# Optimization experiments

Measured on AMD Instinct MI355X. Metric: run time of the kernel, lower is better.

Reference implementation:

```python
import jax, jax.numpy as jnp
import numpy as np

D_MODEL = 384
NUM_CODES = 256
BETAS = (0.05, 0.25, 0.6)
B = 8192


def _vq(x, codebook, beta):
    """Standard EMA-VQ forward: nearest-code lookup + straight-through + commitment loss.
    x: (B, N, D), codebook: (K, D).
    (EMA buffer updates are training-time, no-grad side effects and are omitted.)"""
    flat = x.reshape(-1, x.shape[-1])  # (B*N, D)
    d2 = (jnp.sum(flat * flat, axis=-1, keepdims=True)
          - 2.0 * flat @ codebook.T
          + jnp.sum(codebook * codebook, axis=-1))  # (B*N, K)
    idx = jnp.argmin(d2, axis=-1)                    # (B*N,)
    q_hard = codebook[idx].reshape(x.shape)          # gather (B, N, D)
    idx = idx.reshape(x.shape[:-1])                  # (B, N)
    loss = beta * jnp.mean(jnp.square(jax.lax.stop_gradient(q_hard) - x))
    q = x + jax.lax.stop_gradient(q_hard - x)        # straight-through estimator
    return q, loss, idx


def setup_inputs() -> dict:
    key = jax.random.key(0)
    k0, k1, k2, k3, k4, k5 = jax.random.split(key, 6)
    return {
        "l0_feats": jax.random.normal(k0, (B, 4, D_MODEL), dtype=jnp.float32),
        "l1_feats": jax.random.normal(k1, (B, 16, D_MODEL), dtype=jnp.float32),
        "l2_feats": jax.random.normal(k2, (B, 16, D_MODEL), dtype=jnp.float32),
        "codebook0": jax.random.normal(k3, (NUM_CODES, D_MODEL), dtype=jnp.float32),
        "codebook1": jax.random.normal(k4, (NUM_CODES, D_MODEL), dtype=jnp.float32),
        "codebook2": jax.random.normal(k5, (NUM_CODES, D_MODEL), dtype=jnp.float32),
    }


def reference(l0_feats, l1_feats, l2_feats, codebook0, codebook1, codebook2):
    q0, loss0, idx0 = _vq(l0_feats, codebook0, BETAS[0])
    q1, loss1, idx1 = _vq(l1_feats, codebook1, BETAS[1])
    q2, loss2, idx2 = _vq(l2_feats, codebook2, BETAS[2])
    total_vq_loss = loss0 + loss1 + loss2
    return (idx0, idx1, idx2, total_vq_loss, q0, q1, q2)
```

## Files before the change

### kernel.cpp

```cpp
#include <hip/hip_runtime.h>


typedef _Float16 half8 __attribute__((ext_vector_type(8)));
typedef float f32x16 __attribute__((ext_vector_type(16)));

#define D_MODEL 384
#define NSEG 96
#define NKT 12
#define BM 64
#define RTAU 0.004f

__device__ __forceinline__ float4 ld4(const float* p) { return *(const float4*)p; }

__device__ __forceinline__ void cvt8(const float4& a, const float4& b, half8& hi, half8& lo) {
  const float v[8] = {a.x, a.y, a.z, a.w, b.x, b.y, b.z, b.w};
#pragma unroll
  for (int u = 0; u < 8; ++u) {
    _Float16 h = (_Float16)v[u];
    hi[u] = h;
    lo[u] = (_Float16)(v[u] - (float)h);
  }
}

__device__ __forceinline__ void gload_lds16(const void* g, void* l) {
  __builtin_amdgcn_global_load_lds(
      (const __attribute__((address_space(1))) unsigned int*)g,
      (__attribute__((address_space(3))) unsigned int*)l, 16, 0, 0);
}

__global__ __launch_bounds__(64) void vq_norms(const float* __restrict__ c0,
                                               const float* __restrict__ c1,
                                               const float* __restrict__ c2,
                                               float* __restrict__ en,
                                               int* __restrict__ counts) {
  if (blockIdx.x == 0 && threadIdx.x < 4) counts[threadIdx.x] = 0;
  const int row = blockIdx.x;
  const float* cb = (row < 256) ? c0 : ((row < 512) ? c1 : c2);
  const int n = row & 255;
  const int lane = threadIdx.x;
  const float* r = cb + (size_t)n * D_MODEL;
  float s = 0.f;
  for (int c = lane; c < D_MODEL; c += 64) s = fmaf(r[c], r[c], s);
  for (int m = 1; m < 64; m <<= 1) s += __shfl_xor(s, m, 64);
  if (lane == 0) en[row] = s;
}

__global__ __launch_bounds__(256) void vq_split_cb(const float* __restrict__ c0,
                                                   const float* __restrict__ c1,
                                                   const float* __restrict__ c2,
                                                   half8* __restrict__ bh,
                                                   half8* __restrict__ bl) {
  const int t = blockIdx.x * 256 + threadIdx.x;
  const int lvl = t / 12288;
  const int rem = t - lvl * 12288;
  const int kt = rem >> 10;
  const int f = (rem >> 6) & 15;
  const int lane = rem & 63;
  const int code = (f >> 1) * 32 + (lane & 31);
  const int k0 = kt * 32 + (f & 1) * 16 + (lane >> 5) * 8;
  const float* cb = (lvl == 0) ? c0 : ((lvl == 1) ? c1 : c2);
  const float4 a = ld4(cb + code * D_MODEL + k0);
  const float4 b = ld4(cb + code * D_MODEL + k0 + 4);
  half8 hv, lv;
  cvt8(a, b, hv, lv);
  bh[t] = hv;
  bl[t] = lv;
}

__global__ __launch_bounds__(256) void vq_mfma_all(
    const float* __restrict__ l0, const float* __restrict__ l1,
    const float* __restrict__ l2, const float* __restrict__ c0,
    const float* __restrict__ c1, const float* __restrict__ c2,
    const float* __restrict__ en_all,
    const half8* __restrict__ bh_pre, const half8* __restrict__ bl_pre,
    float* __restrict__ out, float* __restrict__ dmin_all,
    float* __restrict__ xn_all,
    int* __restrict__ list0, int* __restrict__ list1, int* __restrict__ list2,
    int* __restrict__ counts) {
  __shared__ __align__(16) unsigned char smem[40960];
  half8* Ah = (half8*)smem;
  half8* Al = (half8*)(smem + 4096);
  float*  scanbuf = (float*)smem;
  float4* red     = (float4*)(smem + 32768);
  float*  en_s    = (float*)(smem + 36864);
  float4* rowres  = (float4*)(smem + 37888);
  float*  xnp     = (float*)(smem + 38912);
  int*    idxs    = (int*)(smem + 39936);

  const int swz = (blockIdx.x & 7) * 576 + (blockIdx.x >> 3);
  int lvl, blk;
  if (swz < 512)       { lvl = 0; blk = swz; }
  else if (swz < 2560) { lvl = 1; blk = swz - 512; }
  else                 { lvl = 2; blk = swz - 2560; }
  const float* x  = (lvl == 0) ? l0 : ((lvl == 1) ? l1 : l2);
  const float* cb = (lvl == 0) ? c0 : ((lvl == 1) ? c1 : c2);
  const float* en = en_all + lvl * 256;
  const half8* bh = bh_pre + lvl * 12288;
  const half8* bl = bl_pre + lvl * 12288;
  const long ioff = (lvl == 0) ? 0 : ((lvl == 1) ? 32768 : 163840);
  float* out_idx = out + ioff;
  float* out_q   = out + ((lvl == 0) ? 294913L : ((lvl == 1) ? 12877825L : 63209473L));
  float* dmin_lvl = dmin_all + ioff;
  float* xn_lvl   = xn_all + ioff;
  int* list = (lvl == 0) ? list0 : ((lvl == 1) ? list1 : list2);
  int* cnt  = counts + lvl;

  const int tid = threadIdx.x;
  const int lane = tid & 63;
  const int w = tid >> 6, wm = w >> 1, wn = w & 1;
  const int c31 = lane & 31, h = lane >> 5;
  const long m0 = (long)blk * BM;

  const int amt = tid >> 7;
  const int akc = (tid >> 6) & 1;
  const float* ap = x + (m0 + amt * 32 + c31) * (long)D_MODEL + akc * 16 + h * 8;
  const int aidx = (amt * 2 + akc) * 64 + lane;

  float4 ra0 = ld4(ap + 0), ra1 = ld4(ap + 4);

  f32x16 acc[4];
#pragma unroll
  for (int n = 0; n < 4; ++n)
#pragma unroll
    for (int i = 0; i < 16; ++i) acc[n][i] = 0.f;

  float xn_part = 0.f;

  for (int kt = 0; kt < NKT; ++kt) {
#pragma unroll
    for (int r = 0; r < 4; ++r) {
      const int f = r * 4 + w;
      const size_t gi = (size_t)kt * 1024 + f * 64 + lane;
      gload_lds16(bh + gi, (void*)(smem + 8192 + f * 1024));
      gload_lds16(bl + gi, (void*)(smem + 24576 + f * 1024));
    }
    {
      half8 hv, lv;
      cvt8(ra0, ra1, hv, lv);
      xn_part = fmaf(ra0.x, ra0.x, xn_part); xn_part = fmaf(ra0.y, ra0.y, xn_part);
      xn_part = fmaf(ra0.z, ra0.z, xn_part); xn_part = fmaf(ra0.w, ra0.w, xn_part);
      xn_part = fmaf(ra1.x, ra1.x, xn_part); xn_part = fmaf(ra1.y, ra1.y, xn_part);
      xn_part = fmaf(ra1.z, ra1.z, xn_part); xn_part = fmaf(ra1.w, ra1.w, xn_part);
      Ah[aidx] = hv; Al[aidx] = lv;
    }
    __syncthreads();

    if (kt + 1 < NKT) {
      const int ko = (kt + 1) * 32;
      ra0 = ld4(ap + ko); ra1 = ld4(ap + ko + 4);
    }
    {
      half8* Bh = (half8*)(smem + 8192);
      half8* Bl = (half8*)(smem + 24576);
      half8 ah0 = Ah[(wm * 2 + 0) * 64 + lane];
      half8 al0 = Al[(wm * 2 + 0) * 64 + lane];
      half8 ah1 = Ah[(wm * 2 + 1) * 64 + lane];
      half8 al1 = Al[(wm * 2 + 1) * 64 + lane];
#pragma unroll
      for (int n = 0; n < 4; ++n) {
        const int nt = wn * 4 + n;
        half8 bh0 = Bh[(nt * 2 + 0) * 64 + lane], bl0 = Bl[(nt * 2 + 0) * 64 + lane];
        half8 bh1 = Bh[(nt * 2 + 1) * 64 + lane], bl1 = Bl[(nt * 2 + 1) * 64 + lane];
        acc[n] = __builtin_amdgcn_mfma_f32_32x32x16_f16(ah0, bh0, acc[n], 0, 0, 0);
        acc[n] = __builtin_amdgcn_mfma_f32_32x32x16_f16(ah0, bl0, acc[n], 0, 0, 0);
        acc[n] = __builtin_amdgcn_mfma_f32_32x32x16_f16(al0, bh0, acc[n], 0, 0, 0);
        acc[n] = __builtin_amdgcn_mfma_f32_32x32x16_f16(ah1, bh1, acc[n], 0, 0, 0);
        acc[n] = __builtin_amdgcn_mfma_f32_32x32x16_f16(ah1, bl1, acc[n], 0, 0, 0);
        acc[n] = __builtin_amdgcn_mfma_f32_32x32x16_f16(al1, bh1, acc[n], 0, 0, 0);
      }
    }
    __syncthreads();
  }

  xnp[(amt * 32 + c31) * 4 + (akc * 2 + h)] = xn_part;
  en_s[tid] = en[tid];

#pragma unroll 1
  for (int b = 0; b < 2; ++b) {
    __syncthreads();
    if (wm == b) {
#pragma unroll
      for (int n = 0; n < 4; ++n) {
        const int colbase = wn * 128 + n * 32 + c31;
#pragma unroll
        for (int rr = 0; rr < 16; ++rr) {
          const int row_b = (rr & 3) + ((rr >> 2) << 3) + (h << 2);
          const int p = colbase ^ ((row_b & 3) << 3);
          scanbuf[row_b * 256 + p] = fmaf(-2.f, acc[n][rr], en_s[colbase]);
        }
      }
    }
    __syncthreads();
    {
      const int srow = tid >> 3, chunk = tid & 7;
      float b1 = 1e30f, b2 = 1e30f; int i1 = 0, i2 = 0;
#pragma unroll
      for (int u = 0; u < 32; ++u) {
        const int col = chunk + u * 8;
        const float d = scanbuf[srow * 256 + (col ^ ((srow & 3) << 3))];
        if (d < b1) { b2 = b1; i2 = i1; b1 = d; i1 = col; }
        else if (d < b2) { b2 = d; i2 = col; }
      }
      red[srow * 8 + chunk] = make_float4(b1, __int_as_float(i1), b2, __int_as_float(i2));
    }
    __syncthreads();
    if (tid < 32) {
      float4 q = red[tid * 8 + 0];
      float fb1 = q.x, fb2 = q.z;
      int fi1 = __float_as_int(q.y), fi2 = __float_as_int(q.w);
#pragma unroll
      for (int c = 1; c < 8; ++c) {
        q = red[tid * 8 + c];
        const float c1 = q.x, c2 = q.z;
        const int j1 = __float_as_int(q.y), j2 = __float_as_int(q.w);
        if (c1 < fb1 || (c1 == fb1 && j1 < fi1)) {
          if (fb1 < c2 || (fb1 == c2 && fi1 < j2)) { fb2 = fb1; fi2 = fi1; }
          else { fb2 = c2; fi2 = j2; }
          fb1 = c1; fi1 = j1;
        } else if (c1 < fb2 || (c1 == fb2 && j1 < fi2)) { fb2 = c1; fi2 = j1; }
      }
      rowres[b * 32 + tid] = make_float4(fb1, __int_as_float(fi1), fb2, __int_as_float(fi2));
    }
  }
  __syncthreads();

  if (tid < BM) {
    const int m = tid;
    const float4 qv = rowres[m];
    const float fb1 = qv.x, fb2 = qv.z;
    const int fi1 = __float_as_int(qv.y);
    const float xn = (xnp[m * 4 + 0] + xnp[m * 4 + 1]) + (xnp[m * 4 + 2] + xnp[m * 4 + 3]);
    idxs[m] = fi1;
    out_idx[m0 + m] = (float)fi1;
    dmin_lvl[m0 + m] = xn + fb1;
    xn_lvl[m0 + m] = xn;
    const bool flg = (fb2 - fb1 < RTAU);
    const unsigned long long mask = __ballot(flg);
    const int nf = __popcll(mask);
    int base = 0;
    if (tid == 0 && nf) base = atomicAdd(cnt, nf);
    base = __shfl(base, 0, 64);
    if (flg) {
      const int pos = __popcll(mask & ((1ull << tid) - 1ull));
      list[base + pos] = (int)(m0 + m);
    }
  }
  __syncthreads();

  float* qb = out_q + m0 * (long)D_MODEL;
  for (int g = tid; g < BM * NSEG; g += 256) {
    const int m = g / NSEG;
    const int seg = g - m * NSEG;
    *(float4*)(qb + m * (long)D_MODEL + seg * 4) = ld4(cb + (long)idxs[m] * D_MODEL + seg * 4);
  }
}

__global__ __launch_bounds__(256) void vq_rescue_all(
    const float* __restrict__ l0, const float* __restrict__ l1,
    const float* __restrict__ l2, const float* __restrict__ c0,
    const float* __restrict__ c1, const float* __restrict__ c2,
    const float* __restrict__ en_all,
    const int* __restrict__ list0, const int* __restrict__ list1,
    const int* __restrict__ list2, const int* __restrict__ counts,
    float* __restrict__ out, float* __restrict__ dmin_all,
    const float* __restrict__ xn_all) {
  __shared__ float xs[8][D_MODEL];
  __shared__ int rows_s[8];
  __shared__ float xns_s[8];
  __shared__ float dall[8][256];
  __shared__ int best_s[8];

  const int lvl = blockIdx.x >> 7;
  const int sb  = blockIdx.x & 127;
  const float* x  = (lvl == 0) ? l0 : ((lvl == 1) ? l1 : l2);
  const float* cb = (lvl == 0) ? c0 : ((lvl == 1) ? c1 : c2);
  const float* en_lvl = en_all + lvl * 256;
  const int* list = (lvl == 0) ? list0 : ((lvl == 1) ? list1 : list2);
  const long ioff = (lvl == 0) ? 0 : ((lvl == 1) ? 32768 : 163840);
  float* out_idx = out + ioff;
  float* out_q   = out + ((lvl == 0) ? 294913L : ((lvl == 1) ? 12877825L : 63209473L));
  float* dmin_lvl = dmin_all + ioff;
  const float* xn_lvl = xn_all + ioff;

  const int tid = threadIdx.x;
  const int count = counts[lvl];
  const int nch = (count + 7) >> 3;
  const float en_t = en_lvl[tid];
  const int w = tid >> 6, lane = tid & 63;
  const float* crow = cb + (long)tid * D_MODEL;

  for (int c = sb; c < nch; c += 128) {
    const int base = c << 3;
    const int R = min(8, count - base);
    if (tid < 8) {
      const int j = min(tid, R - 1);
      const int r = list[base + j];
      rows_s[tid] = r;
      xns_s[tid] = xn_lvl[r];
    }
    __syncthreads();
#pragma unroll
    for (int r = 0; r < 8; ++r)
      if (tid < NSEG) *(float4*)&xs[r][tid * 4] = ld4(x + (long)rows_s[r] * D_MODEL + tid * 4);
    __syncthreads();

    float acc[8] = {0.f, 0.f, 0.f, 0.f, 0.f, 0.f, 0.f, 0.f};
    for (int seg = 0; seg < NSEG; ++seg) {
      const float4 e = ld4(crow + seg * 4);
#pragma unroll
      for (int r = 0; r < 8; ++r) {
        const float4 xv = *(const float4*)&xs[r][seg * 4];
        acc[r] = fmaf(xv.x, e.x, acc[r]);
        acc[r] = fmaf(xv.y, e.y, acc[r]);
        acc[r] = fmaf(xv.z, e.z, acc[r]);
        acc[r] = fmaf(xv.w, e.w, acc[r]);
      }
    }
#pragma unroll
    for (int r = 0; r < 8; ++r)
      dall[r][tid] = fmaf(-2.f, acc[r], xns_s[r]) + en_t;
    __syncthreads();

#pragma unroll
    for (int rr = 0; rr < 2; ++rr) {
      const int r = w + rr * 4;
      if (r < R) {
        float best = dall[r][lane]; int bidx = lane;
#pragma unroll
        for (int u = 1; u < 4; ++u) {
          const int code = lane + u * 64;
          const float d = dall[r][code];
          if (d < best) { best = d; bidx = code; }
        }
        for (int mm = 1; mm < 64; mm <<= 1) {
          const float ov = __shfl_xor(best, mm, 64);
          const int oi = __shfl_xor(bidx, mm, 64);
          if (ov < best || (ov == best && oi < bidx)) { best = ov; bidx = oi; }
        }
        if (lane == 0) {
          const int row = rows_s[r];
          out_idx[row] = (float)bidx;
          dmin_lvl[row] = best;
          best_s[r] = bidx;
        }
      }
    }
    __syncthreads();
#pragma unroll
    for (int r = 0; r < 8; ++r)
      if (r < R && tid < NSEG)
        *(float4*)(out_q + (long)rows_s[r] * D_MODEL + tid * 4) =
            ld4(cb + (long)best_s[r] * D_MODEL + tid * 4);
    __syncthreads();
  }
}

__global__ __launch_bounds__(256) void loss_stage1(const float* __restrict__ dmin,
                                                   double* __restrict__ lp) {
  const int b = blockIdx.x;
  const int tid = threadIdx.x;
  const long r0 = (long)b * 512;
  __shared__ double sh[256];
  sh[tid] = (double)dmin[r0 + tid] + (double)dmin[r0 + 256 + tid];
  __syncthreads();
  for (int st = 128; st > 0; st >>= 1) {
    if (tid < st) sh[tid] += sh[tid + st];
    __syncthreads();
  }
  if (tid == 0) {
    double scale;
    if (b < 64)       scale = 0.05 / (32768.0 * 384.0);
    else if (b < 320) scale = 0.25 / (131072.0 * 384.0);
    else              scale = 0.60 / (131072.0 * 384.0);
    lp[b] = sh[0] * scale;
  }
}

__global__ __launch_bounds__(256) void loss_stage2(const double* __restrict__ lp,
                                                   float* __restrict__ out_loss) {
  const int tid = threadIdx.x;
  __shared__ double sh[256];
  sh[tid] = lp[tid] + lp[tid + 256] + ((tid < 64) ? lp[tid + 512] : 0.0);
  __syncthreads();
  for (int st = 128; st > 0; st >>= 1) {
    if (tid < st) sh[tid] += sh[tid + st];
    __syncthreads();
  }
  if (tid == 0) out_loss[0] = (float)sh[0];
}

extern "C" void kernel_launch(void* const* d_in, const int* in_sizes, int n_in,
                              void* d_out, int out_size, void* d_ws, size_t ws_size,
                              hipStream_t stream) {
  const float* l0 = (const float*)d_in[0];
  const float* l1 = (const float*)d_in[1];
  const float* l2 = (const float*)d_in[2];
  const float* c0 = (const float*)d_in[3];
  const float* c1 = (const float*)d_in[4];
  const float* c2 = (const float*)d_in[5];
  float* out = (float*)d_out;

  float* wsf = (float*)d_ws;
  int*   counts   = (int*)wsf;
  float* en       = wsf + 4;
  float* dmin_all = wsf + 772;
  float* xn_all   = wsf + 295684;
  int*   list0    = (int*)(wsf + 590596);
  int*   list1    = (int*)(wsf + 623364);
  int*   list2    = (int*)(wsf + 754436);
  double* lp      = (double*)(wsf + 885508);
  half8* bh_pre   = (half8*)(wsf + 886660);
  half8* bl_pre   = (half8*)(wsf + 1034116);

  vq_norms<<<768, 64, 0, stream>>>(c0, c1, c2, en, counts);
  vq_split_cb<<<144, 256, 0, stream>>>(c0, c1, c2, bh_pre, bl_pre);

  vq_mfma_all<<<4608, 256, 0, stream>>>(l0, l1, l2, c0, c1, c2, en,
                                        bh_pre, bl_pre, out,
                                        dmin_all, xn_all,
                                        list0, list1, list2, counts);

  vq_rescue_all<<<384, 256, 0, stream>>>(l0, l1, l2, c0, c1, c2, en,
                                         list0, list1, list2, counts,
                                         out, dmin_all, xn_all);

  loss_stage1<<<576, 256, 0, stream>>>(dmin_all, lp);
  loss_stage2<<<1, 256, 0, stream>>>(lp, out + 294912);
}
```

Before: 428.5 us.

## Double-buffer LDS tiles to overlap next-tile loads with MFMA compute

Shared memory for the x tile and the codebook half/low tiles is split into two ping-pong buffers. The next k-tile's global-to-LDS codebook loads and the x register loads are issued before the current tile is converted and multiplied. Explicit vmcnt/lgkmcnt waits and raw s_barrier calls replace the per-iteration __syncthreads pair, and the k-loop is fully unrolled. The aim is to hide global load latency behind the MFMA work. In exchange, LDS per block doubles to 80 KB, which lowers how many blocks fit on a CU, and the hand-written waitcnt values must match the number of outstanding loads exactly.

```diff
diff --git a/kernel.cpp b/kernel.cpp
--- a/kernel.cpp
+++ b/kernel.cpp
@@ -77,9 +77,7 @@
     float* __restrict__ xn_all,
     int* __restrict__ list0, int* __restrict__ list1, int* __restrict__ list2,
     int* __restrict__ counts) {
-  __shared__ __align__(16) unsigned char smem[40960];
-  half8* Ah = (half8*)smem;
-  half8* Al = (half8*)(smem + 4096);
+  __shared__ __align__(16) unsigned char smem[81920];
   float*  scanbuf = (float*)smem;
   float4* red     = (float4*)(smem + 32768);
   float*  en_s    = (float*)(smem + 36864);
@@ -116,8 +114,6 @@
   const float* ap = x + (m0 + amt * 32 + c31) * (long)D_MODEL + akc * 16 + h * 8;
   const int aidx = (amt * 2 + akc) * 64 + lane;
 
-  float4 ra0 = ld4(ap + 0), ra1 = ld4(ap + 4);
-
   f32x16 acc[4];
 #pragma unroll
   for (int n = 0; n < 4; ++n)
@@ -125,33 +121,56 @@
     for (int i = 0; i < 16; ++i) acc[n][i] = 0.f;
 
   float xn_part = 0.f;
-
+  float4 ra[2][2];
+
+  ra[0][0] = ld4(ap + 0);
+  ra[0][1] = ld4(ap + 4);
+#pragma unroll
+  for (int r = 0; r < 4; ++r) {
+    const int f = r * 4 + w;
+    const size_t gi = (size_t)(f * 64 + lane);
+    gload_lds16(bh + gi, (void*)(smem + 16384 + f * 1024));
+    gload_lds16(bl + gi, (void*)(smem + 16384 + 16384 + f * 1024));
+  }
+
+#pragma unroll
   for (int kt = 0; kt < NKT; ++kt) {
-#pragma unroll
-    for (int r = 0; r < 4; ++r) {
-      const int f = r * 4 + w;
-      const size_t gi = (size_t)kt * 1024 + f * 64 + lane;
-      gload_lds16(bh + gi, (void*)(smem + 8192 + f * 1024));
-      gload_lds16(bl + gi, (void*)(smem + 24576 + f * 1024));
-    }
-    {
-      half8 hv, lv;
-      cvt8(ra0, ra1, hv, lv);
-      xn_part = fmaf(ra0.x, ra0.x, xn_part); xn_part = fmaf(ra0.y, ra0.y, xn_part);
-      xn_part = fmaf(ra0.z, ra0.z, xn_part); xn_part = fmaf(ra0.w, ra0.w, xn_part);
-      xn_part = fmaf(ra1.x, ra1.x, xn_part); xn_part = fmaf(ra1.y, ra1.y, xn_part);
-      xn_part = fmaf(ra1.z, ra1.z, xn_part); xn_part = fmaf(ra1.w, ra1.w, xn_part);
-      Ah[aidx] = hv; Al[aidx] = lv;
-    }
-    __syncthreads();
-
+    const int cur = kt & 1;
+    const int nxt = cur ^ 1;
     if (kt + 1 < NKT) {
       const int ko = (kt + 1) * 32;
-      ra0 = ld4(ap + ko); ra1 = ld4(ap + ko + 4);
+      ra[nxt][0] = ld4(ap + ko);
+      ra[nxt][1] = ld4(ap + ko + 4);
+#pragma unroll
+      for (int r = 0; r < 4; ++r) {
+        const int f = r * 4 + w;
+        const size_t gi = (size_t)(kt + 1) * 1024 + (size_t)(f * 64 + lane);
+        gload_lds16(bh + gi, (void*)(smem + 16384 + nxt * 32768 + f * 1024));
+        gload_lds16(bl + gi, (void*)(smem + 16384 + nxt * 32768 + 16384 + f * 1024));
+      }
     }
     {
-      half8* Bh = (half8*)(smem + 8192);
-      half8* Bl = (half8*)(smem + 24576);
+      const float4 a0 = ra[cur][0], a1 = ra[cur][1];
+      half8 hv, lv;
+      cvt8(a0, a1, hv, lv);
+      xn_part = fmaf(a0.x, a0.x, xn_part); xn_part = fmaf(a0.y, a0.y, xn_part);
+      xn_part = fmaf(a0.z, a0.z, xn_part); xn_part = fmaf(a0.w, a0.w, xn_part);
+      xn_part = fmaf(a1.x, a1.x, xn_part); xn_part = fmaf(a1.y, a1.y, xn_part);
+      xn_part = fmaf(a1.z, a1.z, xn_part); xn_part = fmaf(a1.w, a1.w, xn_part);
+      ((half8*)(smem + cur * 8192))[aidx] = hv;
+      ((half8*)(smem + cur * 8192 + 4096))[aidx] = lv;
+    }
+    if (kt + 1 < NKT) {
+      asm volatile("s_waitcnt vmcnt(10) lgkmcnt(0)" ::: "memory");
+    } else {
+      asm volatile("s_waitcnt vmcnt(0) lgkmcnt(0)" ::: "memory");
+    }
+    __builtin_amdgcn_s_barrier();
+    {
+      const half8* Ah = (const half8*)(smem + cur * 8192);
+      const half8* Al = (const half8*)(smem + cur * 8192 + 4096);
+      const half8* Bh = (const half8*)(smem + 16384 + cur * 32768);
+      const half8* Bl = (const half8*)(smem + 16384 + cur * 32768 + 16384);
       half8 ah0 = Ah[(wm * 2 + 0) * 64 + lane];
       half8 al0 = Al[(wm * 2 + 0) * 64 + lane];
       half8 ah1 = Ah[(wm * 2 + 1) * 64 + lane];
@@ -169,7 +188,7 @@
         acc[n] = __builtin_amdgcn_mfma_f32_32x32x16_f16(al1, bh1, acc[n], 0, 0, 0);
       }
     }
-    __syncthreads();
+    if (kt + 1 < NKT) __builtin_amdgcn_s_barrier();
   }
 
   xnp[(amt * 32 + c31) * 4 + (akc * 2 + h)] = xn_part;
```

After: 398.0 us. -7.1%, faster.

## Drop split-fp16 GEMM to single fp16 with wider rescue margin and fp64 rescue

Applied to the files above, without the earlier changes.

Replaces the three-MFMA hi/lo fp16 split with a single fp16 product, cutting MFMA work and codebook LDS traffic by about a third. A-operand fragments now go straight from registers without LDS staging, and the codebook tiles are double-buffered with one sync per k-step. The rescue threshold grows from 0.004 to 0.5, so many more rows fall into the exact fallback path, which now recomputes distances in fp64. The main risk is that the larger rescue workload and slow fp64 arithmetic offset the GEMM savings.

```diff
diff --git a/kernel.cpp b/kernel.cpp
--- a/kernel.cpp
+++ b/kernel.cpp
@@ -8,18 +8,15 @@
 #define NSEG 96
 #define NKT 12
 #define BM 64
-#define RTAU 0.004f
+#define RTAU 0.5f
 
 __device__ __forceinline__ float4 ld4(const float* p) { return *(const float4*)p; }
 
-__device__ __forceinline__ void cvt8(const float4& a, const float4& b, half8& hi, half8& lo) {
-  const float v[8] = {a.x, a.y, a.z, a.w, b.x, b.y, b.z, b.w};
-#pragma unroll
-  for (int u = 0; u < 8; ++u) {
-    _Float16 h = (_Float16)v[u];
-    hi[u] = h;
-    lo[u] = (_Float16)(v[u] - (float)h);
-  }
+__device__ __forceinline__ half8 cvt8h(const float4& a, const float4& b) {
+  half8 h;
+  h[0] = (_Float16)a.x; h[1] = (_Float16)a.y; h[2] = (_Float16)a.z; h[3] = (_Float16)a.w;
+  h[4] = (_Float16)b.x; h[5] = (_Float16)b.y; h[6] = (_Float16)b.z; h[7] = (_Float16)b.w;
+  return h;
 }
 
 __device__ __forceinline__ void gload_lds16(const void* g, void* l) {
@@ -48,8 +45,7 @@
 __global__ __launch_bounds__(256) void vq_split_cb(const float* __restrict__ c0,
                                                    const float* __restrict__ c1,
                                                    const float* __restrict__ c2,
-                                                   half8* __restrict__ bh,
-                                                   half8* __restrict__ bl) {
+                                                   half8* __restrict__ bh) {
   const int t = blockIdx.x * 256 + threadIdx.x;
   const int lvl = t / 12288;
   const int rem = t - lvl * 12288;
@@ -61,31 +57,26 @@
   const float* cb = (lvl == 0) ? c0 : ((lvl == 1) ? c1 : c2);
   const float4 a = ld4(cb + code * D_MODEL + k0);
   const float4 b = ld4(cb + code * D_MODEL + k0 + 4);
-  half8 hv, lv;
-  cvt8(a, b, hv, lv);
-  bh[t] = hv;
-  bl[t] = lv;
-}
-
-__global__ __launch_bounds__(256) void vq_mfma_all(
+  bh[t] = cvt8h(a, b);
+}
+
+__global__ __launch_bounds__(256, 3) void vq_mfma_all(
     const float* __restrict__ l0, const float* __restrict__ l1,
     const float* __restrict__ l2, const float* __restrict__ c0,
     const float* __restrict__ c1, const float* __restrict__ c2,
     const float* __restrict__ en_all,
-    const half8* __restrict__ bh_pre, const half8* __restrict__ bl_pre,
+    const half8* __restrict__ bh_pre,
     float* __restrict__ out, float* __restrict__ dmin_all,
     float* __restrict__ xn_all,
     int* __restrict__ list0, int* __restrict__ list1, int* __restrict__ list2,
     int* __restrict__ counts) {
   __shared__ __align__(16) unsigned char smem[40960];
-  half8* Ah = (half8*)smem;
-  half8* Al = (half8*)(smem + 4096);
   float*  scanbuf = (float*)smem;
   float4* red     = (float4*)(smem + 32768);
   float*  en_s    = (float*)(smem + 36864);
   float4* rowres  = (float4*)(smem + 37888);
-  float*  xnp     = (float*)(smem + 38912);
-  int*    idxs    = (int*)(smem + 39936);
+  float*  xns     = (float*)(smem + 38912);
+  int*    idxs    = (int*)(smem + 39168);
 
   const int swz = (blockIdx.x & 7) * 576 + (blockIdx.x >> 3);
   int lvl, blk;
@@ -96,7 +87,6 @@
   const float* cb = (lvl == 0) ? c0 : ((lvl == 1) ? c1 : c2);
   const float* en = en_all + lvl * 256;
   const half8* bh = bh_pre + lvl * 12288;
-  const half8* bl = bl_pre + lvl * 12288;
   const long ioff = (lvl == 0) ? 0 : ((lvl == 1) ? 32768 : 163840);
   float* out_idx = out + ioff;
   float* out_q   = out + ((lvl == 0) ? 294913L : ((lvl == 1) ? 12877825L : 63209473L));
@@ -111,12 +101,7 @@
   const int c31 = lane & 31, h = lane >> 5;
   const long m0 = (long)blk * BM;
 
-  const int amt = tid >> 7;
-  const int akc = (tid >> 6) & 1;
-  const float* ap = x + (m0 + amt * 32 + c31) * (long)D_MODEL + akc * 16 + h * 8;
-  const int aidx = (amt * 2 + akc) * 64 + lane;
-
-  float4 ra0 = ld4(ap + 0), ra1 = ld4(ap + 4);
+  const float* ap = x + (m0 + wm * 32 + c31) * (long)D_MODEL + h * 8;
 
   f32x16 acc[4];
 #pragma unroll
@@ -126,53 +111,70 @@
 
   float xn_part = 0.f;
 
+  float4 ra0 = ld4(ap + 0), ra1 = ld4(ap + 4), ra2 = ld4(ap + 16), ra3 = ld4(ap + 20);
+#pragma unroll
+  for (int r = 0; r < 4; ++r) {
+    const int f = r * 4 + w;
+    gload_lds16(bh + (size_t)(f * 64 + lane), (void*)(smem + f * 1024));
+  }
+  xn_part = fmaf(ra0.x, ra0.x, xn_part); xn_part = fmaf(ra0.y, ra0.y, xn_part);
+  xn_part = fmaf(ra0.z, ra0.z, xn_part); xn_part = fmaf(ra0.w, ra0.w, xn_part);
+  xn_part = fmaf(ra1.x, ra1.x, xn_part); xn_part = fmaf(ra1.y, ra1.y, xn_part);
+  xn_part = fmaf(ra1.z, ra1.z, xn_part); xn_part = fmaf(ra1.w, ra1.w, xn_part);
+  xn_part = fmaf(ra2.x, ra2.x, xn_part); xn_part = fmaf(ra2.y, ra2.y, xn_part);
+  xn_part = fmaf(ra2.z, ra2.z, xn_part); xn_part = fmaf(ra2.w, ra2.w, xn_part);
+  xn_part = fmaf(ra3.x, ra3.x, xn_part); xn_part = fmaf(ra3.y, ra3.y, xn_part);
+  xn_part = fmaf(ra3.z, ra3.z, xn_part); xn_part = fmaf(ra3.w, ra3.w, xn_part);
+  half8 ahc0 = cvt8h(ra0, ra1);
+  half8 ahc1 = cvt8h(ra2, ra3);
+  __syncthreads();
+
+#pragma unroll
   for (int kt = 0; kt < NKT; ++kt) {
-#pragma unroll
-    for (int r = 0; r < 4; ++r) {
-      const int f = r * 4 + w;
-      const size_t gi = (size_t)kt * 1024 + f * 64 + lane;
-      gload_lds16(bh + gi, (void*)(smem + 8192 + f * 1024));
-      gload_lds16(bl + gi, (void*)(smem + 24576 + f * 1024));
+    const int cur = kt & 1;
+    const int nxt = cur ^ 1;
+    float4 rb0, rb1, rb2, rb3;
+    if (kt + 1 < NKT) {
+#pragma unroll
+      for (int r = 0; r < 4; ++r) {
+        const int f = r * 4 + w;
+        gload_lds16(bh + (size_t)(kt + 1) * 1024 + (size_t)(f * 64 + lane),
+                    (void*)(smem + nxt * 16384 + f * 1024));
+      }
+      const int ko = (kt + 1) * 32;
+      rb0 = ld4(ap + ko); rb1 = ld4(ap + ko + 4);
+      rb2 = ld4(ap + ko + 16); rb3 = ld4(ap + ko + 20);
     }
     {
-      half8 hv, lv;
-      cvt8(ra0, ra1, hv, lv);
-      xn_part = fmaf(ra0.x, ra0.x, xn_part); xn_part = fmaf(ra0.y, ra0.y, xn_part);
-      xn_part = fmaf(ra0.z, ra0.z, xn_part); xn_part = fmaf(ra0.w, ra0.w, xn_part);
-      xn_part = fmaf(ra1.x, ra1.x, xn_part); xn_part = fmaf(ra1.y, ra1.y, xn_part);
-      xn_part = fmaf(ra1.z, ra1.z, xn_part); xn_part = fmaf(ra1.w, ra1.w, xn_part);
-      Ah[aidx] = hv; Al[aidx] = lv;
-    }
-    __syncthreads();
-
-    if (kt + 1 < NKT) {
-      const int ko = (kt + 1) * 32;
-      ra0 = ld4(ap + ko); ra1 = ld4(ap + ko + 4);
-    }
-    {
-      half8* Bh = (half8*)(smem + 8192);
-      half8* Bl = (half8*)(smem + 24576);
-      half8 ah0 = Ah[(wm * 2 + 0) * 64 + lane];
-      half8 al0 = Al[(wm * 2 + 0) * 64 + lane];
-      half8 ah1 = Ah[(wm * 2 + 1) * 64 + lane];
-      half8 al1 = Al[(wm * 2 + 1) * 64 + lane];
+      const half8* Bh = (const half8*)(smem + cur * 16384);
 #pragma unroll
       for (int n = 0; n < 4; ++n) {
         const int nt = wn * 4 + n;
-        half8 bh0 = Bh[(nt * 2 + 0) * 64 + lane], bl0 = Bl[(nt * 2 + 0) * 64 + lane];
-        half8 bh1 = Bh[(nt * 2 + 1) * 64 + lane], bl1 = Bl[(nt * 2 + 1) * 64 + lane];
-        acc[n] = __builtin_amdgcn_mfma_f32_32x32x16_f16(ah0, bh0, acc[n], 0, 0, 0);
-        acc[n] = __builtin_amdgcn_mfma_f32_32x32x16_f16(ah0, bl0, acc[n], 0, 0, 0);
-        acc[n] = __builtin_amdgcn_mfma_f32_32x32x16_f16(al0, bh0, acc[n], 0, 0, 0);
-        acc[n] = __builtin_amdgcn_mfma_f32_32x32x16_f16(ah1, bh1, acc[n], 0, 0, 0);
-        acc[n] = __builtin_amdgcn_mfma_f32_32x32x16_f16(ah1, bl1, acc[n], 0, 0, 0);
-        acc[n] = __builtin_amdgcn_mfma_f32_32x32x16_f16(al1, bh1, acc[n], 0, 0, 0);
-      }
-    }
-    __syncthreads();
-  }
-
-  xnp[(amt * 32 + c31) * 4 + (akc * 2 + h)] = xn_part;
+        half8 b0 = Bh[(nt * 2 + 0) * 64 + lane];
+        half8 b1 = Bh[(nt * 2 + 1) * 64 + lane];
+        acc[n] = __builtin_amdgcn_mfma_f32_32x32x16_f16(ahc0, b0, acc[n], 0, 0, 0);
+        acc[n] = __builtin_amdgcn_mfma_f32_32x32x16_f16(ahc1, b1, acc[n], 0, 0, 0);
+      }
+    }
+    if (kt + 1 < NKT) {
+      xn_part = fmaf(rb0.x, rb0.x, xn_part); xn_part = fmaf(rb0.y, rb0.y, xn_part);
+      xn_part = fmaf(rb0.z, rb0.z, xn_part); xn_part = fmaf(rb0.w, rb0.w, xn_part);
+      xn_part = fmaf(rb1.x, rb1.x, xn_part); xn_part = fmaf(rb1.y, rb1.y, xn_part);
+      xn_part = fmaf(rb1.z, rb1.z, xn_part); xn_part = fmaf(rb1.w, rb1.w, xn_part);
+      xn_part = fmaf(rb2.x, rb2.x, xn_part); xn_part = fmaf(rb2.y, rb2.y, xn_part);
+      xn_part = fmaf(rb2.z, rb2.z, xn_part); xn_part = fmaf(rb2.w, rb2.w, xn_part);
+      xn_part = fmaf(rb3.x, rb3.x, xn_part); xn_part = fmaf(rb3.y, rb3.y, xn_part);
+      xn_part = fmaf(rb3.z, rb3.z, xn_part); xn_part = fmaf(rb3.w, rb3.w, xn_part);
+      ahc0 = cvt8h(rb0, rb1);
+      ahc1 = cvt8h(rb2, rb3);
+      __syncthreads();
+    }
+  }
+
+  {
+    const float xr = xn_part + __shfl_xor(xn_part, 32, 64);
+    if (wn == 0 && lane < 32) xns[wm * 32 + lane] = xr;
+  }
   en_s[tid] = en[tid];
 
 #pragma unroll 1
@@ -229,7 +231,7 @@
     const float4 qv = rowres[m];
     const float fb1 = qv.x, fb2 = qv.z;
     const int fi1 = __float_as_int(qv.y);
-    const float xn = (xnp[m * 4 + 0] + xnp[m * 4 + 1]) + (xnp[m * 4 + 2] + xnp[m * 4 + 3]);
+    const float xn = xns[m];
     idxs[m] = fi1;
     out_idx[m0 + m] = (float)fi1;
     dmin_lvl[m0 + m] = xn + fb1;
@@ -265,16 +267,15 @@
     float* __restrict__ out, float* __restrict__ dmin_all,
     const float* __restrict__ xn_all) {
   __shared__ float xs[8][D_MODEL];
+  __shared__ double dall[8][256];
   __shared__ int rows_s[8];
   __shared__ float xns_s[8];
-  __shared__ float dall[8][256];
   __shared__ int best_s[8];
 
   const int lvl = blockIdx.x >> 7;
   const int sb  = blockIdx.x & 127;
   const float* x  = (lvl == 0) ? l0 : ((lvl == 1) ? l1 : l2);
   const float* cb = (lvl == 0) ? c0 : ((lvl == 1) ? c1 : c2);
-  const float* en_lvl = en_all + lvl * 256;
   const int* list = (lvl == 0) ? list0 : ((lvl == 1) ? list1 : list2);
   const long ioff = (lvl == 0) ? 0 : ((lvl == 1) ? 32768 : 163840);
   float* out_idx = out + ioff;
@@ -285,7 +286,6 @@
   const int tid = threadIdx.x;
   const int count = counts[lvl];
   const int nch = (count + 7) >> 3;
-  const float en_t = en_lvl[tid];
   const int w = tid >> 6, lane = tid & 63;
   const float* crow = cb + (long)tid * D_MODEL;
 
@@ -304,43 +304,40 @@
       if (tid < NSEG) *(float4*)&xs[r][tid * 4] = ld4(x + (long)rows_s[r] * D_MODEL + tid * 4);
     __syncthreads();
 
-    float acc[8] = {0.f, 0.f, 0.f, 0.f, 0.f, 0.f, 0.f, 0.f};
-    for (int seg = 0; seg < NSEG; ++seg) {
-      const float4 e = ld4(crow + seg * 4);
-#pragma unroll
-      for (int r = 0; r < 8; ++r) {
-        const float4 xv = *(const float4*)&xs[r][seg * 4];
-        acc[r] = fmaf(xv.x, e.x, acc[r]);
-        acc[r] = fmaf(xv.y, e.y, acc[r]);
-        acc[r] = fmaf(xv.z, e.z, acc[r]);
-        acc[r] = fmaf(xv.w, e.w, acc[r]);
-      }
+    double en_d = 0.0;
+    double dot[8] = {0.0, 0.0, 0.0, 0.0, 0.0, 0.0, 0.0, 0.0};
+    for (int k = 0; k < D_MODEL; ++k) {
+      const double cd = (double)crow[k];
+      en_d = fma(cd, cd, en_d);
+#pragma unroll
+      for (int r = 0; r < 8; ++r)
+        dot[r] = fma(cd, (double)xs[r][k], dot[r]);
     }
 #pragma unroll
     for (int r = 0; r < 8; ++r)
-      dall[r][tid] = fmaf(-2.f, acc[r], xns_s[r]) + en_t;
+      dall[r][tid] = fma(-2.0, dot[r], en_d);
     __syncthreads();
 
 #pragma unroll
     for (int rr = 0; rr < 2; ++rr) {
       const int r = w + rr * 4;
       if (r < R) {
-        float best = dall[r][lane]; int bidx = lane;
+        double best = dall[r][lane]; int bidx = lane;
 #pragma unroll
         for (int u = 1; u < 4; ++u) {
           const int code = lane + u * 64;
-          const float d = dall[r][code];
+          const double d = dall[r][code];
           if (d < best) { best = d; bidx = code; }
         }
         for (int mm = 1; mm < 64; mm <<= 1) {
-          const float ov = __shfl_xor(best, mm, 64);
+          const double ov = __shfl_xor(best, mm, 64);
           const int oi = __shfl_xor(bidx, mm, 64);
           if (ov < best || (ov == best && oi < bidx)) { best = ov; bidx = oi; }
         }
         if (lane == 0) {
           const int row = rows_s[r];
           out_idx[row] = (float)bidx;
-          dmin_lvl[row] = best;
+          dmin_lvl[row] = xns_s[r] + (float)best;
           best_s[r] = bidx;
         }
       }
@@ -410,13 +407,12 @@
   int*   list2    = (int*)(wsf + 754436);
   double* lp      = (double*)(wsf + 885508);
   half8* bh_pre   = (half8*)(wsf + 886660);
-  half8* bl_pre   = (half8*)(wsf + 1034116);
 
   vq_norms<<<768, 64, 0, stream>>>(c0, c1, c2, en, counts);
-  vq_split_cb<<<144, 256, 0, stream>>>(c0, c1, c2, bh_pre, bl_pre);
+  vq_split_cb<<<144, 256, 0, stream>>>(c0, c1, c2, bh_pre);
 
   vq_mfma_all<<<4608, 256, 0, stream>>>(l0, l1, l2, c0, c1, c2, en,
-                                        bh_pre, bl_pre, out,
+                                        bh_pre, out,
                                         dmin_all, xn_all,
                                         list0, list1, list2, counts);
 
```

Result: slower. 482.0 us (+12.5%).
